# Kernel optimization log

Measured on AMD Instinct MI355X. Metric: run time of the kernel, lower is better.

Reference implementation:

```python
import math
import jax, jax.numpy as jnp
import numpy as np

ALPH = 0.8

def setup_inputs() -> dict:
    key = jax.random.key(0)
    k1, k2 = jax.random.split(key)
    B, C, N, T = 64, 64, 500, 48
    x = jax.random.normal(k1, (B, C, N, T), dtype=jnp.float32)
    s = jax.random.uniform(k2, (N, N), dtype=jnp.float32)
    return {"x": x, "s": s}

def reference(x, s):
    # x: [B, C, N, T], s: [N, N]
    B, C, N, T = x.shape
    # Row sums of the (never materialized) [N*T, N*T] supra-laplacian:
    # block row i, node v -> s.sum(axis=1)[v] + (T-1-i)*alph
    s_rowsum = s.sum(axis=1)                              # [N]
    time_term = (T - 1 - jnp.arange(T, dtype=jnp.float32)) * ALPH  # [T]
    rowsum = (time_term[:, None] + s_rowsum[None, :]).reshape(-1)  # [T*N], k = i*N+v
    # Faithful to original: x flattened as [B, C, N*T] (k = n*T + t), multiplied
    # elementwise by rowsum[k] (the 'bcn,nm->bcn' einsum reduces to this).
    x_window = x.reshape(B, C, N * T)
    x_window = jax.nn.relu(x_window * rowsum / math.sqrt(C))
    adj_dyn = jax.nn.softmax(x_window, axis=-1)            # [B, C, N*T]
    x_w_s = adj_dyn.reshape(B, C, N, T).sum(-1)            # [B, C, N]
    gram = jnp.einsum('bcn,bcm->bnm', x_w_s, x_w_s)        # [B, N, N]
    A_l = jax.nn.softmax(jax.nn.relu(gram) / math.sqrt(C), axis=-1)
    return A_l
```

## Files before the change

### kernel.cpp

```cpp
#include <hip/hip_runtime.h>
#include <math.h>

#define NN 500
#define TT 48
#define NT 24000
#define NF4 6000

typedef float f4v __attribute__((ext_vector_type(4)));

__global__ void k_srow(const float* __restrict__ s, float* __restrict__ srow) {
    int r = blockIdx.x;
    int l = threadIdx.x;
    float v = 0.f;
    for (int j = l; j < NN; j += 64) v += s[r * NN + j];
    #pragma unroll
    for (int o = 32; o; o >>= 1) v += __shfl_xor(v, o);
    if (l == 0) srow[r] = v;
}

__launch_bounds__(256, 8)
__global__ void k_p1(const float* __restrict__ x, const float* __restrict__ srow,
                     float* __restrict__ xraw, float* __restrict__ mz) {
    __shared__ float p[3072];
    __shared__ __align__(16) float sr[512];
    int bid = blockIdx.x;
    int bc = bid >> 1, half = bid & 1;
    int tid = threadIdx.x;
    int w = tid >> 6, l = tid & 63;
    int fl0 = w * 768 + l;
    int f0 = half * 3072 + fl0;

    sr[tid] = srow[(tid < NN) ? tid : (NN - 1)];
    int t2 = tid + 256;
    sr[t2] = (t2 < NN) ? srow[t2] : 0.f;
    __syncthreads();

    const f4v* xp = (const f4v*)x + (size_t)bc * NF4;

    float sf[12], ml[12];
    float m = 0.f;
    #pragma unroll
    for (int i = 0; i < 12; i++) {
        int f = f0 + i * 64;
        int fc = (f < NF4) ? f : (NF4 - 1);
        float msk = (f < NF4) ? 1.f : 0.f;
        f4v xv = xp[fc];
        int kk = 4 * fc;
        int ti = kk / 500;
        int v  = kk - ti * 500;
        float tt = (float)(TT - 1 - ti) * 0.8f;
        float4 sv = *(const float4*)(sr + v);
        float y0 = fmaxf(xv.x * (tt + sv.x) * 0.125f, 0.f);
        float y1 = fmaxf(xv.y * (tt + sv.y) * 0.125f, 0.f);
        float y2 = fmaxf(xv.z * (tt + sv.z) * 0.125f, 0.f);
        float y3 = fmaxf(xv.w * (tt + sv.w) * 0.125f, 0.f);
        float mm = fmaxf(fmaxf(y0, y1), fmaxf(y2, y3));
        float sfi = __expf(y0 - mm) + __expf(y1 - mm)
                  + __expf(y2 - mm) + __expf(y3 - mm);
        sf[i] = sfi * msk;
        ml[i] = mm;
        m = fmaxf(m, mm);
    }
    #pragma unroll
    for (int o = 32; o; o >>= 1) m = fmaxf(m, __shfl_xor(m, o));

    float tot = 0.f;
    #pragma unroll
    for (int i = 0; i < 12; i++) {
        float cf = sf[i] * __expf(ml[i] - m);
        p[fl0 + i * 64] = cf;
        tot += cf;
    }
    #pragma unroll
    for (int o = 32; o; o >>= 1) tot += __shfl_xor(tot, o);

    asm volatile("s_waitcnt lgkmcnt(0)" ::: "memory");

    int n = half * 256 + w * 64 + l;
    if (n < NN) {
        const float4* pp = (const float4*)(p + w * 768 + l * 12);
        float4 a = pp[0], b4 = pp[1], c4 = pp[2];
        float sn = a.x + a.y + a.z + a.w + b4.x + b4.y + b4.z + b4.w
                 + c4.x + c4.y + c4.z + c4.w;
        xraw[(size_t)bc * NN + n] = sn;
    }
    if (l == 0) {
        int wv = half * 4 + w;
        mz[((size_t)bc * 8 + wv) * 2 + 0] = m;
        mz[((size_t)bc * 8 + wv) * 2 + 1] = tot;
    }
}

__global__ void k_mz(const float* __restrict__ mz, float* __restrict__ factor) {
    int bc = blockIdx.x * 256 + threadIdx.x;
    float Mw[8], Zw[8];
    float M = 0.f;
    #pragma unroll
    for (int wv = 0; wv < 8; wv++) {
        Mw[wv] = mz[((size_t)bc * 8 + wv) * 2 + 0];
        Zw[wv] = mz[((size_t)bc * 8 + wv) * 2 + 1];
        M = fmaxf(M, Mw[wv]);
    }
    float Z = 0.f;
    float e[8];
    #pragma unroll
    for (int wv = 0; wv < 8; wv++) {
        e[wv] = __expf(Mw[wv] - M);
        Z += Zw[wv] * e[wv];
    }
    float invZ = 1.f / Z;
    #pragma unroll
    for (int wv = 0; wv < 8; wv++)
        factor[(size_t)bc * 8 + wv] = e[wv] * invZ;
}

__launch_bounds__(512, 4)
__global__ void k_p2(const float* __restrict__ xraw, const float* __restrict__ factor,
                     float* __restrict__ out) {
    __shared__ __align__(16) float Xs[32 * NN + 16];
    int b = blockIdx.y;
    int rt8 = blockIdx.x;
    int tid = threadIdx.x;

    int rt = tid >> 6, cx = tid & 63;
    int r0 = rt8 * 64 + rt * 8;
    int cb0 = cx * 4, cb1 = cx * 4 + 256;

    float acc[8][8];
    #pragma unroll
    for (int i = 0; i < 8; i++)
        #pragma unroll
        for (int j = 0; j < 8; j++) acc[i][j] = 0.f;

    for (int cbk = 0; cbk < 2; cbk++) {
        const float4* src4 = (const float4*)(xraw + ((size_t)b * 64 + 32 * cbk) * NN);
        const float* fac = factor + ((size_t)b * 64 + 32 * cbk) * 8;
        __syncthreads();
        #pragma unroll
        for (int i = 0; i < 8; i++) {
            int idx = tid + i * 512;
            if (idx < 4000) {
                int c = idx / 125;
                int n4 = idx - c * 125;
                float fct = fac[c * 8 + (n4 >> 4)];
                float4 v = src4[idx];
                v.x *= fct; v.y *= fct; v.z *= fct; v.w *= fct;
                ((float4*)Xs)[idx] = v;
            }
        }
        if (tid < 16) Xs[32 * NN + tid] = 0.f;
        __syncthreads();

        #pragma unroll 4
        for (int c = 0; c < 32; c++) {
            const float* row = Xs + c * NN;
            float4 a0 = *(const float4*)(row + r0);
            float4 a1 = *(const float4*)(row + r0 + 4);
            float4 b0 = *(const float4*)(row + cb0);
            float4 b1 = *(const float4*)(row + cb1);
            float av[8] = {a0.x, a0.y, a0.z, a0.w, a1.x, a1.y, a1.z, a1.w};
            float bv[8] = {b0.x, b0.y, b0.z, b0.w, b1.x, b1.y, b1.z, b1.w};
            #pragma unroll
            for (int i = 0; i < 8; i++)
                #pragma unroll
                for (int j = 0; j < 8; j++)
                    acc[i][j] = fmaf(av[i], bv[j], acc[i][j]);
        }
    }

    bool c1v = (cx <= 60);
    size_t ob = (size_t)b * (NN * NN);
    #pragma unroll 1
    for (int ri = 0; ri < 8; ri++) {
        int r = r0 + ri;
        if (r >= NN) break;
        float u[8];
        #pragma unroll
        for (int j = 0; j < 8; j++) u[j] = fmaxf(acc[ri][j], 0.f) * 0.125f;
        float mx = fmaxf(fmaxf(u[0], u[1]), fmaxf(u[2], u[3]));
        if (c1v) mx = fmaxf(mx, fmaxf(fmaxf(u[4], u[5]), fmaxf(u[6], u[7])));
        #pragma unroll
        for (int o = 32; o; o >>= 1) mx = fmaxf(mx, __shfl_xor(mx, o));

        float e[8];
        float es = 0.f;
        #pragma unroll
        for (int j = 0; j < 4; j++) { e[j] = __expf(u[j] - mx); es += e[j]; }
        if (c1v) {
            #pragma unroll
            for (int j = 4; j < 8; j++) { e[j] = __expf(u[j] - mx); es += e[j]; }
        }
        #pragma unroll
        for (int o = 32; o; o >>= 1) es += __shfl_xor(es, o);
        float inv = 1.f / es;

        float4 w0 = make_float4(e[0] * inv, e[1] * inv, e[2] * inv, e[3] * inv);
        *(float4*)(out + ob + (size_t)r * NN + cb0) = w0;
        if (c1v) {
            float4 w1 = make_float4(e[4] * inv, e[5] * inv, e[6] * inv, e[7] * inv);
            *(float4*)(out + ob + (size_t)r * NN + cb1) = w1;
        }
    }
}

extern "C" void kernel_launch(void* const* d_in, const int* in_sizes, int n_in,
                              void* d_out, int out_size, void* d_ws, size_t ws_size,
                              hipStream_t stream) {
    const float* x = (const float*)d_in[0];
    const float* s = (const float*)d_in[1];
    float* out = (float*)d_out;
    float* wsf = (float*)d_ws;

    float* srow   = wsf;
    float* xraw   = wsf + 32768;
    float* mz     = wsf + 32768 + 2048000;
    float* factor = wsf + 32768 + 2048000 + 65536;

    k_srow<<<NN, 64, 0, stream>>>(s, srow);
    k_p1<<<64 * 64 * 2, 256, 0, stream>>>(x, srow, xraw, mz);
    k_mz<<<16, 256, 0, stream>>>(mz, factor);
    dim3 g2(8, 64);
    k_p2<<<g2, 512, 0, stream>>>(xraw, factor, out);
}
```

Before: 167.4 us.

## Stage x loads through LDS with async global_load_lds double buffering in k_p1

Measured after the change: 165.3 us. No clear change (-1.2%).

```diff
diff --git a/kernel.cpp b/kernel.cpp
--- a/kernel.cpp
+++ b/kernel.cpp
@@ -18,17 +18,18 @@
     if (l == 0) srow[r] = v;
 }
 
-__launch_bounds__(256, 8)
+__launch_bounds__(256, 4)
 __global__ void k_p1(const float* __restrict__ x, const float* __restrict__ srow,
                      float* __restrict__ xraw, float* __restrict__ mz) {
     __shared__ float p[3072];
     __shared__ __align__(16) float sr[512];
+    __shared__ __align__(16) float stg[4][2][768];
     int bid = blockIdx.x;
     int bc = bid >> 1, half = bid & 1;
     int tid = threadIdx.x;
     int w = tid >> 6, l = tid & 63;
     int fl0 = w * 768 + l;
-    int f0 = half * 3072 + fl0;
+    int rowb = half * 3072 + w * 768;
 
     sr[tid] = srow[(tid < NN) ? tid : (NN - 1)];
     int t2 = tid + 256;
@@ -37,30 +38,65 @@
 
     const f4v* xp = (const f4v*)x + (size_t)bc * NF4;
 
+#define STAGE(s) do {                                                         \
+        _Pragma("unroll")                                                     \
+        for (int k_ = 0; k_ < 3; k_++) {                                      \
+            int f_ = rowb + (s) * 192 + k_ * 64 + l;                          \
+            int fc_ = (f_ < NF4) ? f_ : (NF4 - 1);                            \
+            __builtin_amdgcn_global_load_lds(                                 \
+                (const __attribute__((address_space(1))) void*)(xp + fc_),    \
+                (__attribute__((address_space(3))) void*)&stg[w][(s) & 1][k_ * 256], \
+                16, 0, 0);                                                    \
+        }                                                                     \
+    } while (0)
+
+#define VMCNT(n) do {                                                         \
+        asm volatile("s_waitcnt vmcnt(" #n ")" ::: "memory");                 \
+        __builtin_amdgcn_sched_barrier(0);                                    \
+    } while (0)
+
     float sf[12], ml[12];
     float m = 0.f;
-    #pragma unroll
-    for (int i = 0; i < 12; i++) {
-        int f = f0 + i * 64;
-        int fc = (f < NF4) ? f : (NF4 - 1);
-        float msk = (f < NF4) ? 1.f : 0.f;
-        f4v xv = xp[fc];
-        int kk = 4 * fc;
-        int ti = kk / 500;
-        int v  = kk - ti * 500;
-        float tt = (float)(TT - 1 - ti) * 0.8f;
-        float4 sv = *(const float4*)(sr + v);
-        float y0 = fmaxf(xv.x * (tt + sv.x) * 0.125f, 0.f);
-        float y1 = fmaxf(xv.y * (tt + sv.y) * 0.125f, 0.f);
-        float y2 = fmaxf(xv.z * (tt + sv.z) * 0.125f, 0.f);
-        float y3 = fmaxf(xv.w * (tt + sv.w) * 0.125f, 0.f);
-        float mm = fmaxf(fmaxf(y0, y1), fmaxf(y2, y3));
-        float sfi = __expf(y0 - mm) + __expf(y1 - mm)
-                  + __expf(y2 - mm) + __expf(y3 - mm);
-        sf[i] = sfi * msk;
-        ml[i] = mm;
-        m = fmaxf(m, mm);
-    }
+
+#define COMPU(s) do {                                                         \
+        _Pragma("unroll")                                                     \
+        for (int k_ = 0; k_ < 3; k_++) {                                      \
+            int i_ = 3 * (s) + k_;                                            \
+            int f_ = rowb + (s) * 192 + k_ * 64 + l;                          \
+            int fc_ = (f_ < NF4) ? f_ : (NF4 - 1);                            \
+            float msk_ = (f_ < NF4) ? 1.f : 0.f;                              \
+            float4 xv = ((const float4*)stg[w][(s) & 1])[k_ * 64 + l];        \
+            int kk_ = 4 * fc_;                                                \
+            int ti_ = kk_ / 500;                                              \
+            int v_  = kk_ - ti_ * 500;                                        \
+            float tt_ = (float)(TT - 1 - ti_) * 0.8f;                         \
+            float4 sv = *(const float4*)(sr + v_);                            \
+            float y0 = fmaxf(xv.x * (tt_ + sv.x) * 0.125f, 0.f);              \
+            float y1 = fmaxf(xv.y * (tt_ + sv.y) * 0.125f, 0.f);              \
+            float y2 = fmaxf(xv.z * (tt_ + sv.z) * 0.125f, 0.f);              \
+            float y3 = fmaxf(xv.w * (tt_ + sv.w) * 0.125f, 0.f);              \
+            float mm_ = fmaxf(fmaxf(y0, y1), fmaxf(y2, y3));                  \
+            float sfi_ = __expf(y0 - mm_) + __expf(y1 - mm_)                  \
+                       + __expf(y2 - mm_) + __expf(y3 - mm_);                 \
+            sf[i_] = sfi_ * msk_;                                             \
+            ml[i_] = mm_;                                                     \
+            m = fmaxf(m, mm_);                                                \
+        }                                                                     \
+    } while (0)
+
+    STAGE(0);
+    STAGE(1);
+    VMCNT(3);  COMPU(0);
+    STAGE(2);
+    VMCNT(3);  COMPU(1);
+    STAGE(3);
+    VMCNT(3);  COMPU(2);
+    VMCNT(0);  COMPU(3);
+
+#undef STAGE
+#undef VMCNT
+#undef COMPU
+
     #pragma unroll
     for (int o = 32; o; o >>= 1) m = fmaxf(m, __shfl_xor(m, o));
 
@@ -75,6 +111,7 @@
     for (int o = 32; o; o >>= 1) tot += __shfl_xor(tot, o);
 
     asm volatile("s_waitcnt lgkmcnt(0)" ::: "memory");
+    __builtin_amdgcn_sched_barrier(0);
 
     int n = half * 256 + w * 64 + l;
     if (n < NN) {
```
